# Performance work log

Hardware: AMD Instinct MI355X
Metric: run time of the kernel (lower is better)

## Reference

```python
import jax, jax.numpy as jnp
import numpy as np

WINDOW = 21
PATCH = 1
H_PARAM = 0.1
EPS = 1e-10


def _box_sum(x, w):
    # Sum over a w x w sliding window (VALID), per (batch, channel).
    return jax.lax.reduce_window(x, 0.0, jax.lax.add,
                                 (1, 1, w, w), (1, 1, 1, 1), 'VALID')


def setup_inputs() -> dict:
    key = jax.random.key(0)
    noisy = jax.random.uniform(key, (8, 3, 512, 512), dtype=jnp.float32)
    return {"noisy": noisy}


def reference(noisy) -> jnp.ndarray:
    # Faithful vectorization of the per-pixel loop for patch_size=1.
    # For each pixel p=(i,j):
    #   window = padded[i:i+W, j:j+W]; center = noisy[i,j]
    #   dists  = mean((window - center)^2)
    #   weights = exp(-dists / h^2)            # shape (B, C)
    #   patch  = window[0, 0] = padded[i, j]   # top-left of window (half_patch=0)
    #   out[:, c, i, j] = sum_b weights[b,c] * patch[b,c]   (sum over BATCH)
    #   wsum[:, c, i, j] = sum_b weights[b,c]
    # out = clamp(out / (wsum + 1e-10), 0, 1)
    h2 = H_PARAM * H_PARAM
    W = WINDOW
    pad = W // 2
    B, C, Hh, Ww = noisy.shape
    padded = jnp.pad(noisy, ((0, 0), (0, 0), (pad, pad), (pad, pad)), mode='reflect')

    # mean((window - center)^2) = (S2 - 2*center*S1 + W^2*center^2) / W^2
    s1 = _box_sum(padded, W)                  # (B, C, H, W)
    s2 = _box_sum(padded * padded, W)
    n_win = jnp.asarray(W * W, dtype=noisy.dtype)
    dists = (s2 - 2.0 * noisy * s1 + n_win * noisy * noisy) / n_win

    weights = jnp.exp(-dists / h2)            # (B, C, H, W)
    patch = padded[:, :, :Hh, :Ww]            # top-left pixel of each window

    num = jnp.sum(weights * patch, axis=0, keepdims=True)   # (1, C, H, W)
    den = jnp.sum(weights, axis=0, keepdims=True)
    out = num / (den + EPS)
    out = jnp.broadcast_to(out, noisy.shape)  # loop assigns same row to all b
    return jnp.clip(out, 0.0, 1.0)
```

## Files before the change

### kernel.cpp

```cpp
#include <hip/hip_runtime.h>

#define B 8
#define CCH 3
#define HH 512
#define WW 512
#define WIN 21
#define PAD 10
#define TSX 32
#define TSY 32
#define PTY 52
#define TROW 60
#define HSH 53
#define NSLOT 676

__global__ __launch_bounds__(256, 3) void nlm_fused_kernel(const float* __restrict__ noisy,
                                                           float* __restrict__ out) {
    __shared__ float  tile[2][PTY][TROW];
    __shared__ float2 hs_t[2][TSX][HSH];

    const int tid = threadIdx.x;
    const int x0 = blockIdx.x * TSX;
    const int y0 = blockIdx.y * TSY;
    const int ch = blockIdx.z;

    int   rowbase[3], gxs[3], lr[3], lc[3];
    bool  valid[3], edge[3];
    #pragma unroll
    for (int k = 0; k < 3; ++k) {
        int s = tid + 256 * k;
        valid[k] = (s < NSLOT);
        int ss = valid[k] ? s : 0;
        int r  = ss / 13;
        int c4 = ss - r * 13;
        int gy = y0 + r - PAD;
        gy = (gy < 0) ? -gy : ((gy >= HH) ? (2 * (HH - 1) - gy) : gy);
        int gx = x0 + (c4 << 2) - PAD;
        rowbase[k] = gy * WW;
        gxs[k]     = gx;
        edge[k]    = (gx < 0) || (gx > WW - 4);
        lr[k]      = r;
        lc[k]      = c4 << 2;
    }

    float4 pre[3];
    auto prefetch = [&](int bb) {
        const float* src = noisy + (size_t)(bb * CCH + ch) * (HH * WW);
        #pragma unroll
        for (int k = 0; k < 3; ++k) {
            if (valid[k]) {
                if (!edge[k]) {
                    pre[k] = *(const float4*)(src + rowbase[k] + gxs[k]);
                } else {
                    float tmp[4];
                    #pragma unroll
                    for (int t = 0; t < 4; ++t) {
                        int gx = gxs[k] + t;
                        gx = (gx < 0) ? -gx : ((gx >= WW) ? (2 * (WW - 1) - gx) : gx);
                        tmp[t] = src[rowbase[k] + gx];
                    }
                    pre[k] = make_float4(tmp[0], tmp[1], tmp[2], tmp[3]);
                }
            }
        }
    };

    prefetch(0);
    #pragma unroll
    for (int k = 0; k < 3; ++k)
        if (valid[k]) *(float4*)&tile[0][lr[k]][lc[k]] = pre[k];
    prefetch(1);
    __syncthreads();

    float num[4] = {0.f, 0.f, 0.f, 0.f};
    float den[4] = {0.f, 0.f, 0.f, 0.f};

    const int tx  = tid & 31;
    const int ty0 = (tid >> 5) << 2;
    const int hr  = tid >> 2;
    const int hc0 = (tid & 3) << 3;

    for (int b = 0; b < B; ++b) {
        const int cur = b & 1;
        if (hr < PTY) {
            float v[28];
            #pragma unroll
            for (int q = 0; q < 7; ++q)
                *(float4*)&v[q * 4] = *(const float4*)&tile[cur][hr][hc0 + (q << 2)];
            float s1 = 0.f, s2 = 0.f;
            #pragma unroll
            for (int k = 0; k <= 20; ++k) { s1 += v[k]; s2 = fmaf(v[k], v[k], s2); }
            hs_t[cur][hc0][hr] = make_float2(s1, s2);
            #pragma unroll
            for (int j = 1; j < 8; ++j) {
                float vo = v[j - 1], vn = v[j + 20];
                s1 += vn - vo;
                s2 += vn * vn - vo * vo;
                hs_t[cur][hc0 + j][hr] = make_float2(s1, s2);
            }
        }
        __syncthreads();

        if (b < B - 1) {
            #pragma unroll
            for (int k = 0; k < 3; ++k)
                if (valid[k]) *(float4*)&tile[1 - cur][lr[k]][lc[k]] = pre[k];
            if (b < B - 2) prefetch(b + 2);
        }

        float2 h0 = hs_t[cur][tx][ty0];
        float2 h1 = hs_t[cur][tx][ty0 + 1];
        float2 h2 = hs_t[cur][tx][ty0 + 2];
        float vs1 = h0.x + h1.x + h2.x;
        float vs2 = h0.y + h1.y + h2.y;
        #pragma unroll
        for (int k = 3; k <= 20; ++k) {
            float2 h = hs_t[cur][tx][ty0 + k];
            vs1 += h.x;
            vs2 += h.y;
        }
        const float kE = (-100.0f / 441.0f) * 1.44269504088896f;
        {
            float a = tile[cur][ty0 + PAD][tx + PAD];
            float p = tile[cur][ty0][tx];
            float dd = fmaf(a, fmaf(441.f, a, -2.f * vs1), vs2);
            float w = exp2f(dd * kE);
            num[0] += w * p; den[0] += w;
        }
        #pragma unroll
        for (int i = 1; i < 4; ++i) {
            float2 hn = hs_t[cur][tx][ty0 + 20 + i];
            float2 ho = (i == 1) ? h0 : ((i == 2) ? h1 : h2);
            vs1 += hn.x - ho.x;
            vs2 += hn.y - ho.y;
            float a = tile[cur][ty0 + i + PAD][tx + PAD];
            float p = tile[cur][ty0 + i][tx];
            float dd = fmaf(a, fmaf(441.f, a, -2.f * vs1), vs2);
            float w = exp2f(dd * kE);
            num[i] += w * p; den[i] += w;
        }
        if (b < B - 1) __syncthreads();
    }

    #pragma unroll
    for (int i = 0; i < 4; ++i) {
        int y = y0 + ty0 + i;
        int x = x0 + tx;
        float v = num[i] / (den[i] + 1e-10f);
        v = v < 0.f ? 0.f : (v > 1.f ? 1.f : v);
        #pragma unroll
        for (int b = 0; b < B; ++b)
            out[((size_t)(b * CCH + ch) * HH + y) * WW + x] = v;
    }
}

extern "C" void kernel_launch(void* const* d_in, const int* in_sizes, int n_in,
                              void* d_out, int out_size, void* d_ws, size_t ws_size,
                              hipStream_t stream) {
    const float* noisy = (const float*)d_in[0];
    float* out = (float*)d_out;
    dim3 grid(WW / TSX, HH / TSY, CCH);
    nlm_fused_kernel<<<grid, dim3(256), 0, stream>>>(noisy, out);
}
```

Baseline: 90.55 us.

## Halve block size, single-buffer LDS, and give each thread more output rows

Drops the block from 256 to 128 threads. Each thread now computes 8 output rows and 16 horizontal prefix columns instead of 4 and 8, and the double-buffered LDS tile is replaced by a single buffer with register prefetch of the next batch. The center and top-left pixel values are read straight from global memory instead of from LDS. This cuts LDS footprint and raises per-thread work, trading more redundant global loads and an extra barrier per batch for fewer threads and better reuse of the vertical running sums.

```diff
diff --git a/kernel.cpp b/kernel.cpp
--- a/kernel.cpp
+++ b/kernel.cpp
@@ -4,7 +4,6 @@
 #define CCH 3
 #define HH 512
 #define WW 512
-#define WIN 21
 #define PAD 10
 #define TSX 32
 #define TSY 32
@@ -12,22 +11,25 @@
 #define TROW 60
 #define HSH 53
 #define NSLOT 676
+#define NT 128
+#define NPRE 6
 
-__global__ __launch_bounds__(256, 3) void nlm_fused_kernel(const float* __restrict__ noisy,
-                                                           float* __restrict__ out) {
-    __shared__ float  tile[2][PTY][TROW];
-    __shared__ float2 hs_t[2][TSX][HSH];
+__global__ __launch_bounds__(NT) void nlm_fused_kernel(const float* __restrict__ noisy,
+                                                       float* __restrict__ out) {
+    __shared__ float  tile[PTY][TROW];
+    __shared__ float2 hs_t[TSX][HSH];
 
     const int tid = threadIdx.x;
     const int x0 = blockIdx.x * TSX;
     const int y0 = blockIdx.y * TSY;
     const int ch = blockIdx.z;
 
-    int   rowbase[3], gxs[3], lr[3], lc[3];
-    bool  valid[3], edge[3];
+    int   rowbase[NPRE], gxs[NPRE];
+    float* ldsp[NPRE];
+    bool  valid[NPRE], edge[NPRE];
     #pragma unroll
-    for (int k = 0; k < 3; ++k) {
-        int s = tid + 256 * k;
+    for (int k = 0; k < NPRE; ++k) {
+        int s = tid + NT * k;
         valid[k] = (s < NSLOT);
         int ss = valid[k] ? s : 0;
         int r  = ss / 13;
@@ -38,15 +40,14 @@
         rowbase[k] = gy * WW;
         gxs[k]     = gx;
         edge[k]    = (gx < 0) || (gx > WW - 4);
-        lr[k]      = r;
-        lc[k]      = c4 << 2;
+        ldsp[k]    = &tile[r][c4 << 2];
     }
 
-    float4 pre[3];
+    float4 pre[NPRE];
     auto prefetch = [&](int bb) {
         const float* src = noisy + (size_t)(bb * CCH + ch) * (HH * WW);
         #pragma unroll
-        for (int k = 0; k < 3; ++k) {
+        for (int k = 0; k < NPRE; ++k) {
             if (valid[k]) {
                 if (!edge[k]) {
                     pre[k] = *(const float4*)(src + rowbase[k] + gxs[k]);
@@ -64,87 +65,93 @@
         }
     };
 
+    const int tx  = tid & 31;
+    const int ty0 = (tid >> 5) << 3;
+    const int x   = x0 + tx;
+    int px = x - PAD;  px = (px < 0) ? -px : px;
+    const int a_base = (y0 + ty0) * WW + x;
+    int p_off[8];
+    #pragma unroll
+    for (int i = 0; i < 8; ++i) {
+        int py = y0 + ty0 + i - PAD;
+        py = (py < 0) ? -py : py;
+        p_off[i] = py * WW + px;
+    }
+
+    const int hrow = tid >> 1;
+    const int hseg = (tid & 1) << 4;
+
+    float num[8], den[8];
+    #pragma unroll
+    for (int i = 0; i < 8; ++i) { num[i] = 0.f; den[i] = 0.f; }
+
     prefetch(0);
-    #pragma unroll
-    for (int k = 0; k < 3; ++k)
-        if (valid[k]) *(float4*)&tile[0][lr[k]][lc[k]] = pre[k];
-    prefetch(1);
-    __syncthreads();
-
-    float num[4] = {0.f, 0.f, 0.f, 0.f};
-    float den[4] = {0.f, 0.f, 0.f, 0.f};
-
-    const int tx  = tid & 31;
-    const int ty0 = (tid >> 5) << 2;
-    const int hr  = tid >> 2;
-    const int hc0 = (tid & 3) << 3;
 
     for (int b = 0; b < B; ++b) {
-        const int cur = b & 1;
-        if (hr < PTY) {
-            float v[28];
+        const float* src = noisy + (size_t)(b * CCH + ch) * (HH * WW);
+        __syncthreads();
+        #pragma unroll
+        for (int k = 0; k < NPRE; ++k)
+            if (valid[k]) *(float4*)ldsp[k] = pre[k];
+        __syncthreads();
+
+        if (b < B - 1) prefetch(b + 1);
+
+        float av[8], pv[8];
+        #pragma unroll
+        for (int i = 0; i < 8; ++i) {
+            av[i] = src[a_base + i * WW];
+            pv[i] = src[p_off[i]];
+        }
+
+        if (tid < PTY * 2) {
+            float v[36];
             #pragma unroll
-            for (int q = 0; q < 7; ++q)
-                *(float4*)&v[q * 4] = *(const float4*)&tile[cur][hr][hc0 + (q << 2)];
+            for (int q = 0; q < 9; ++q)
+                *(float4*)&v[q * 4] = *(const float4*)&tile[hrow][hseg + (q << 2)];
             float s1 = 0.f, s2 = 0.f;
             #pragma unroll
             for (int k = 0; k <= 20; ++k) { s1 += v[k]; s2 = fmaf(v[k], v[k], s2); }
-            hs_t[cur][hc0][hr] = make_float2(s1, s2);
+            hs_t[hseg][hrow] = make_float2(s1, s2);
             #pragma unroll
-            for (int j = 1; j < 8; ++j) {
+            for (int j = 1; j < 16; ++j) {
                 float vo = v[j - 1], vn = v[j + 20];
                 s1 += vn - vo;
                 s2 += vn * vn - vo * vo;
-                hs_t[cur][hc0 + j][hr] = make_float2(s1, s2);
+                hs_t[hseg + j][hrow] = make_float2(s1, s2);
             }
         }
         __syncthreads();
 
-        if (b < B - 1) {
-            #pragma unroll
-            for (int k = 0; k < 3; ++k)
-                if (valid[k]) *(float4*)&tile[1 - cur][lr[k]][lc[k]] = pre[k];
-            if (b < B - 2) prefetch(b + 2);
-        }
+        float2 hh[21];
+        #pragma unroll
+        for (int k = 0; k < 21; ++k) hh[k] = hs_t[tx][ty0 + k];
+        float vs1 = 0.f, vs2 = 0.f;
+        #pragma unroll
+        for (int k = 0; k < 21; ++k) { vs1 += hh[k].x; vs2 += hh[k].y; }
 
-        float2 h0 = hs_t[cur][tx][ty0];
-        float2 h1 = hs_t[cur][tx][ty0 + 1];
-        float2 h2 = hs_t[cur][tx][ty0 + 2];
-        float vs1 = h0.x + h1.x + h2.x;
-        float vs2 = h0.y + h1.y + h2.y;
-        #pragma unroll
-        for (int k = 3; k <= 20; ++k) {
-            float2 h = hs_t[cur][tx][ty0 + k];
-            vs1 += h.x;
-            vs2 += h.y;
-        }
         const float kE = (-100.0f / 441.0f) * 1.44269504088896f;
         {
-            float a = tile[cur][ty0 + PAD][tx + PAD];
-            float p = tile[cur][ty0][tx];
+            float a = av[0];
             float dd = fmaf(a, fmaf(441.f, a, -2.f * vs1), vs2);
             float w = exp2f(dd * kE);
-            num[0] += w * p; den[0] += w;
+            num[0] += w * pv[0]; den[0] += w;
         }
         #pragma unroll
-        for (int i = 1; i < 4; ++i) {
-            float2 hn = hs_t[cur][tx][ty0 + 20 + i];
-            float2 ho = (i == 1) ? h0 : ((i == 2) ? h1 : h2);
-            vs1 += hn.x - ho.x;
-            vs2 += hn.y - ho.y;
-            float a = tile[cur][ty0 + i + PAD][tx + PAD];
-            float p = tile[cur][ty0 + i][tx];
+        for (int i = 1; i < 8; ++i) {
+            float2 hn = hs_t[tx][ty0 + 20 + i];
+            vs1 += hn.x - hh[i - 1].x;
+            vs2 += hn.y - hh[i - 1].y;
+            float a = av[i];
             float dd = fmaf(a, fmaf(441.f, a, -2.f * vs1), vs2);
             float w = exp2f(dd * kE);
-            num[i] += w * p; den[i] += w;
+            num[i] += w * pv[i]; den[i] += w;
         }
-        if (b < B - 1) __syncthreads();
     }
 
     #pragma unroll
-    for (int i = 0; i < 4; ++i) {
+    for (int i = 0; i < 8; ++i) {
         int y = y0 + ty0 + i;
-        int x = x0 + tx;
         float v = num[i] / (den[i] + 1e-10f);
         v = v < 0.f ? 0.f : (v > 1.f ? 1.f : v);
         #pragma unroll
@@ -159,5 +166,5 @@
     const float* noisy = (const float*)d_in[0];
     float* out = (float*)d_out;
     dim3 grid(WW / TSX, HH / TSY, CCH);
-    nlm_fused_kernel<<<grid, dim3(256), 0, stream>>>(noisy, out);
+    nlm_fused_kernel<<<grid, dim3(NT), 0, stream>>>(noisy, out);
 }
```

Measured after the change: 90.02 us. About the same (-0.6%).
